# Performance work log

Measured on AMD Instinct MI355X. Metric: run time of the kernel, lower is better.

Reference implementation:

```python
import jax, jax.numpy as jnp
import numpy as np

LN_EPS = 1e-6          # flax nn.LayerNorm default
ATTN_EPS = 1e-9        # numerical_stabilizer default


def ln_points(x, scale, bias):
    """flax LayerNorm(reduction_axes=-2): stats over points axis, affine over feature axis."""
    mu = jnp.mean(x, axis=-2, keepdims=True)
    var = jnp.mean(jnp.square(x), axis=-2, keepdims=True) - jnp.square(mu)
    return (x - mu) * jax.lax.rsqrt(var + LN_EPS) * scale + bias


def self_attention_layer(x, wq_i, bq_i, wk_i, bk_i, wv_i, bv_i, wo_i, bo_i, ls_i, lb_i):
    # 1x1 convs == pointwise linears
    q = x @ wq_i + bq_i                                  # [B,N,C]
    k = x @ wk_i + bk_i
    v = x @ wv_i + bv_i
    attn = jnp.einsum('bmc,bnc->bmn', q, k)              # [B,M,N]
    attn = jax.nn.softmax(attn, axis=-1)
    # extra offset-attention renorm: divide by column sums (axis=1)
    attn = attn / (ATTN_EPS + jnp.sum(attn, axis=1, keepdims=True))
    # einsum '...MN,...NC->...NC' reduces M: scales v by column sums
    col = jnp.sum(attn, axis=1)                          # [B,N]
    out = col[..., None] * v                             # [B,N,C]
    out = out @ wo_i + bo_i
    out = jax.nn.relu(ln_points(out, ls_i, lb_i))
    return out + x


def setup_inputs() -> dict:
    key = jax.random.key(0)
    ks = jax.random.split(key, 16)
    B, N, IN, C, F, L = 2, 4096, 3, 256, 1024, 4
    s_in = 1.0 / np.sqrt(IN)
    s_c = 1.0 / np.sqrt(C)
    s_f = 1.0 / np.sqrt(L * C)
    return {
        'inputs': jax.random.normal(ks[0], (B, N, IN), jnp.float32),
        'w0': jax.random.normal(ks[1], (IN, C), jnp.float32) * s_in,
        'b0': jnp.zeros((C,), jnp.float32),
        'ln0_s': jnp.ones((C,), jnp.float32),
        'ln0_b': jnp.zeros((C,), jnp.float32),
        'w1': jax.random.normal(ks[2], (C, C), jnp.float32) * s_c,
        'b1': jnp.zeros((C,), jnp.float32),
        'ln1_s': jnp.ones((C,), jnp.float32),
        'ln1_b': jnp.zeros((C,), jnp.float32),
        'wq': jax.random.normal(ks[3], (L, C, C), jnp.float32) * s_c,
        'bq': jnp.zeros((L, C), jnp.float32),
        'wk': jax.random.normal(ks[4], (L, C, C), jnp.float32) * s_c,
        'bk': jnp.zeros((L, C), jnp.float32),
        'wv': jax.random.normal(ks[5], (L, C, C), jnp.float32) * s_c,
        'bv': jnp.zeros((L, C), jnp.float32),
        'wo': jax.random.normal(ks[6], (L, C, C), jnp.float32) * s_c,
        'bo': jnp.zeros((L, C), jnp.float32),
        'attn_ln_s': jnp.ones((L, C), jnp.float32),
        'attn_ln_b': jnp.zeros((L, C), jnp.float32),
        'wf': jax.random.normal(ks[7], (L * C, F), jnp.float32) * s_f,
        'bf': jnp.zeros((F,), jnp.float32),
    }


def reference(inputs, w0, b0, ln0_s, ln0_b, w1, b1, ln1_s, ln1_b,
              wq, bq, wk, bk, wv, bv, wo, bo, attn_ln_s, attn_ln_b, wf, bf):
    # pre-conv stack
    out = ln_points(inputs @ w0 + b0, ln0_s, ln0_b)
    out = ln_points(out @ w1 + b1, ln1_s, ln1_b)
    # attention stack (4 structurally identical layers, concatenated)
    attn_outs = []
    for i in range(wq.shape[0]):
        out = self_attention_layer(out, wq[i], bq[i], wk[i], bk[i],
                                   wv[i], bv[i], wo[i], bo[i],
                                   attn_ln_s[i], attn_ln_b[i])
        attn_outs.append(out)
    out = jnp.concatenate(attn_outs, axis=-1)            # [B,N,4C]
    out = out @ wf + bf                                  # [B,N,F]
    return out
```

## Files before the change

### kernel.cpp

```cpp
#include <hip/hip_runtime.h>

#define BB 2
#define NN 4096
#define CC 256
#define FF 1024
#define NLAYER 4
#define RR (BB*NN)
#define SPL 16
#define QKLD (3*CC)
#define NEG_BIG (-1e30f)
#define LOG2E 1.44269504f

typedef _Float16 h16;
typedef __attribute__((ext_vector_type(8))) _Float16 half8;
typedef __attribute__((ext_vector_type(4))) float f32x4;
typedef __attribute__((ext_vector_type(16))) float f32x16;

#define WAITVM4 asm volatile("s_waitcnt vmcnt(4)" ::: "memory")
#define WAITVM0 asm volatile("s_waitcnt vmcnt(0)" ::: "memory")

__device__ __forceinline__ void gload16(const h16* g, h16* l) {
    __builtin_amdgcn_global_load_lds((const __attribute__((address_space(1))) void*)g,
                                     (__attribute__((address_space(3))) void*)l, 16, 0, 0);
}

template<int ROWS>
__device__ __forceinline__ void stage_rows(const h16* __restrict__ src, int ld,
    int row0, int c0, h16* lds, int tid)
{
    int w = tid >> 6;
    #pragma unroll
    for (int t = 0; t < ROWS/32; ++t) {
        int slot = t*256 + tid;
        int row = slot >> 3;
        int pp  = slot & 7;
        int piece = pp ^ (row & 7);
        gload16(src + (size_t)(row0 + row)*ld + c0 + piece*8,
                lds + (t*256 + w*64)*8);
    }
}

__device__ __forceinline__ half8 frag_ld(const h16* lds, int row, int pl) {
    return *(const half8*)(lds + row*64 + ((pl ^ (row & 7))*8));
}

__global__ __launch_bounds__(256) void pct_wtrans(const float* __restrict__ W,
    h16* __restrict__ WT, int K, int N, int dstride, float scale)
{
    __shared__ h16 t[32][33];
    const float* Wl = W + (size_t)blockIdx.z*K*N;
    h16* WTl = WT + (size_t)blockIdx.z*dstride;
    int k0 = blockIdx.x*32, n0 = blockIdx.y*32;
    int tx = threadIdx.x & 31, ty = threadIdx.x >> 5;
    #pragma unroll
    for (int i = ty; i < 32; i += 8)
        t[i][tx] = (h16)(Wl[(size_t)(k0+i)*N + n0 + tx] * scale);
    __syncthreads();
    #pragma unroll
    for (int i = ty; i < 32; i += 8)
        WTl[(size_t)(n0+i)*K + k0 + tx] = t[tx][i];
}

__global__ __launch_bounds__(256) void pct_wtrans_qkv(const float* __restrict__ wq,
    const float* __restrict__ wk, const float* __restrict__ wv, h16* __restrict__ WT)
{
    __shared__ h16 t[32][33];
    int z = blockIdx.z;
    int which = z >> 2, layer = z & 3;
    const float* Wl = (which == 0 ? wq : which == 1 ? wk : wv) + (size_t)layer*CC*CC;
    h16* WTl = WT + (size_t)layer*QKLD*CC + (size_t)which*CC*CC;
    float scale = (which == 0) ? LOG2E : 1.0f;
    int k0 = blockIdx.x*32, n0 = blockIdx.y*32;
    int tx = threadIdx.x & 31, ty = threadIdx.x >> 5;
    #pragma unroll
    for (int i = ty; i < 32; i += 8)
        t[i][tx] = (h16)(Wl[(size_t)(k0+i)*CC + n0 + tx] * scale);
    __syncthreads();
    #pragma unroll
    for (int i = ty; i < 32; i += 8)
        WTl[(size_t)(n0+i)*CC + k0 + tx] = t[tx][i];
}

__global__ __launch_bounds__(256) void pct_bias3(const float* __restrict__ bq,
    const float* __restrict__ bk, const float* __restrict__ bv, float* __restrict__ o)
{
    int l = blockIdx.x, c = threadIdx.x;
    o[l*QKLD + c]        = bq[l*CC + c] * LOG2E;
    o[l*QKLD + CC + c]   = bk[l*CC + c];
    o[l*QKLD + 2*CC + c] = bv[l*CC + c];
}

__global__ __launch_bounds__(256) void pct_embed(const float* __restrict__ inp,
    const float* __restrict__ w0, const float* __restrict__ b0,
    h16* __restrict__ out, float* __restrict__ sums)
{
    int c = threadIdx.x;
    int r0 = blockIdx.x * 64;
    float wa = w0[c], wb = w0[CC+c], wcv = w0[2*CC+c], bb = b0[c];
    float s1 = 0.f, s2 = 0.f;
    #pragma unroll 4
    for (int i = 0; i < 64; ++i) {
        int r = r0 + i;
        float y = bb + inp[r*3+0]*wa + inp[r*3+1]*wb + inp[r*3+2]*wcv;
        h16 hy = (h16)y;
        out[(size_t)r*CC + c] = hy;
        float yf = (float)hy;
        s1 += yf; s2 += yf*yf;
    }
    int b = r0 >> 12;
    atomicAdd(&sums[((size_t)b*CC + c)*2 + 0], s1);
    atomicAdd(&sums[((size_t)b*CC + c)*2 + 1], s2);
}

__global__ __launch_bounds__(256) void pct_lnapply(const h16* __restrict__ x, int ldx,
    const float* __restrict__ sums, const float* __restrict__ scale, const float* __restrict__ bias,
    const h16* __restrict__ res, int ldr, h16* __restrict__ out, int ldo,
    int do_relu)
{
    int r = blockIdx.x*8 + (threadIdx.x >> 5);
    int cg = (threadIdx.x & 31) * 8;
    int b = r / NN;
    half8 xv = *(const half8*)(x + (size_t)r*ldx + cg);
    half8 rv;
    if (res) rv = *(const half8*)(res + (size_t)r*ldr + cg);
    half8 ov;
    #pragma unroll
    for (int j = 0; j < 8; ++j) {
        int c = cg + j;
        float s1 = sums[(b*CC + c)*2], s2 = sums[(b*CC + c)*2 + 1];
        float mu  = s1 * (1.f/NN);
        float var = s2 * (1.f/NN) - mu*mu;
        float rstd = rsqrtf(var + 1e-6f);
        float y = ((float)xv[j] - mu) * rstd * scale[c] + bias[c];
        if (do_relu) y = fmaxf(y, 0.f);
        if (res) y += (float)rv[j];
        ov[j] = (h16)y;
    }
    *(half8*)(out + (size_t)r*ldo + cg) = ov;
}

template<int BN, bool OUT_F32, bool CSTAT>
__global__ __launch_bounds__(256) void pct_gemm_f16(
    const h16* __restrict__ A, int lda,
    const h16* __restrict__ WT, const float* __restrict__ bias,
    void* __restrict__ outp, int ldo, int K, const float* __restrict__ rowS,
    float* __restrict__ csums)
{
    constexpr int BJ = BN/2;
    constexpr int NF = BJ/16;
    __shared__ __align__(16) h16 Asm[128*64];
    __shared__ __align__(16) h16 Bsm[BN*64];
    const int tid = threadIdx.x;
    const int lane = tid & 63, w = tid >> 6;
    const int ln = lane & 15, lq = lane >> 4;
    const int wr = w >> 1, wc = w & 1;
    const int m0 = blockIdx.x*128, n0 = blockIdx.y*BN;
    f32x4 acc[4][NF];
    #pragma unroll
    for (int i = 0; i < 4; ++i)
        #pragma unroll
        for (int j = 0; j < NF; ++j) acc[i][j] = (f32x4){0.f,0.f,0.f,0.f};
    for (int k0 = 0; k0 < K; k0 += 64) {
        stage_rows<128>(A, lda, m0, k0, Asm, tid);
        stage_rows<BN>(WT, K, n0, k0, Bsm, tid);
        __syncthreads();
        #pragma unroll
        for (int kk = 0; kk < 2; ++kk) {
            half8 af[4], bfr[NF];
            #pragma unroll
            for (int i = 0; i < 4; ++i) af[i] = frag_ld(Asm, wr*64 + i*16 + ln, kk*4 + lq);
            #pragma unroll
            for (int j = 0; j < NF; ++j) bfr[j] = frag_ld(Bsm, wc*BJ + j*16 + ln, kk*4 + lq);
            #pragma unroll
            for (int i = 0; i < 4; ++i)
                #pragma unroll
                for (int j = 0; j < NF; ++j)
                    acc[i][j] = __builtin_amdgcn_mfma_f32_16x16x32_f16(af[i], bfr[j], acc[i][j], 0, 0, 0);
        }
        __syncthreads();
    }
    float cs1[NF], cs2[NF];
    #pragma unroll
    for (int j = 0; j < NF; ++j) {
        int col = n0 + wc*BJ + j*16 + ln;
        float bv = bias[col];
        float s1 = 0.f, s2 = 0.f;
        #pragma unroll
        for (int i = 0; i < 4; ++i) {
            #pragma unroll
            for (int r = 0; r < 4; ++r) {
                int row = m0 + wr*64 + i*16 + lq*4 + r;
                float sc = 1.f;
                if (rowS) { float s = rowS[row]; sc = s / (1e-9f + s); }
                float v = acc[i][j][r] * sc + bv;
                if (OUT_F32) ((float*)outp)[(size_t)row*ldo + col] = v;
                else ((h16*)outp)[(size_t)row*ldo + col] = (h16)v;
                if (CSTAT) { s1 += v; s2 += v*v; }
            }
        }
        cs1[j] = s1; cs2[j] = s2;
    }
    if constexpr (CSTAT) {
        __shared__ float cred[2][2][BJ][2];
        #pragma unroll
        for (int j = 0; j < NF; ++j) {
            float s1 = cs1[j], s2 = cs2[j];
            s1 += __shfl_down(s1, 16); s1 += __shfl_down(s1, 32);
            s2 += __shfl_down(s2, 16); s2 += __shfl_down(s2, 32);
            if (lane < 16) {
                cred[wr][wc][j*16 + lane][0] = s1;
                cred[wr][wc][j*16 + lane][1] = s2;
            }
        }
        __syncthreads();
        if (tid < 2*BN) {
            int c = tid >> 1, st = tid & 1;
            int wcc = c >> 5, ci = c & 31;
            float v = cred[0][wcc][ci][st] + cred[1][wcc][ci][st];
            int b = m0 >> 12;
            atomicAdd(&csums[((size_t)b*CC + n0 + c)*2 + st], v);
        }
    }
}

__global__ __launch_bounds__(256) void attn_rowstats(const h16* __restrict__ QKV,
    float2* __restrict__ part)
{
    __shared__ __align__(16) h16 Ks[3*128*64];
    const int b = blockIdx.x, mt = blockIdx.y, sp = blockIdx.z;
    const int tid = threadIdx.x;
    const int lane = tid & 63, w = tid >> 6;
    const int ln2 = lane & 31, h = lane >> 5;
    const h16* qb = QKV + (size_t)b*NN*QKLD;
    const h16* kb = qb + CC;
    const int m0 = mt*128;
    const h16* qrow = qb + (size_t)(m0 + w*32 + ln2)*QKLD + h*8;
    half8 qreg[16];
    #pragma unroll
    for (int i = 0; i < 16; ++i) qreg[i] = *(const half8*)(qrow + i*16);

    const int nbeg = sp*(NN/SPL);
    constexpr int NT = (NN/SPL)/128;
    constexpr int NCH = NT*4;
    float rm = NEG_BIG, rs = 0.f;

    stage_rows<128>(kb, QKLD, nbeg, 0, Ks, tid);
    stage_rows<128>(kb, QKLD, nbeg, 64, Ks + 8192, tid);
    int id = 0;
    #pragma unroll
    for (int t = 0; t < NT; ++t) {
        f32x16 acc[4];
        #pragma unroll
        for (int j = 0; j < 4; ++j) acc[j] = (f32x16)(0.f);
        #pragma unroll
        for (int c = 0; c < 4; ++c, ++id) {
            if (id == NCH-1) { WAITVM0; } else { WAITVM4; }
            __builtin_amdgcn_s_barrier();
            if (id + 2 < NCH)
                stage_rows<128>(kb, QKLD, nbeg + ((id+2) >> 2)*128, ((id+2) & 3)*64,
                                Ks + ((id+2) % 3)*8192, tid);
            const h16* buf = Ks + (id % 3)*8192;
            __builtin_amdgcn_s_setprio(1);
            #pragma unroll
            for (int kk = 0; kk < 4; ++kk) {
                half8 bq = qreg[c*4 + kk];
                #pragma unroll
                for (int j = 0; j < 4; ++j) {
                    half8 af = frag_ld(buf, j*32 + ln2, kk*2 + h);
                    acc[j] = __builtin_amdgcn_mfma_f32_32x32x16_f16(af, bq, acc[j], 0, 0, 0);
                }
            }
            __builtin_amdgcn_s_setprio(0);
        }
        float tm = NEG_BIG;
        #pragma unroll
        for (int j = 0; j < 4; ++j)
            #pragma unroll
            for (int g = 0; g < 16; g += 2)
                tm = fmaxf(tm, fmaxf(acc[j][g], acc[j][g+1]));
        if (tm > rm) { rs *= exp2f(rm - tm); rm = tm; }
        float s = 0.f;
        #pragma unroll
        for (int j = 0; j < 4; ++j)
            #pragma unroll
            for (int g = 0; g < 16; ++g)
                s += exp2f(acc[j][g] - rm);
        rs += s;
    }
    float mo = __shfl_xor(rm, 32, 64);
    float so = __shfl_xor(rs, 32, 64);
    float mn = fmaxf(rm, mo);
    float sm = rs*exp2f(rm - mn) + so*exp2f(mo - mn);
    if (lane < 32) {
        int m = m0 + w*32 + ln2;
        part[((size_t)b*NN + m)*SPL + sp] = make_float2(mn, sm);
    }
}

__global__ __launch_bounds__(256) void attn_colsums(const h16* __restrict__ QKV,
    const float2* __restrict__ part, float* __restrict__ S)
{
    __shared__ __align__(16) h16 Qs[3*128*64];
    __shared__ float2 rst_s[256];
    const int b = blockIdx.x, nt = blockIdx.y, sp = blockIdx.z;
    const int tid = threadIdx.x;
    const int lane = tid & 63, w = tid >> 6;
    const int ln2 = lane & 31, h = lane >> 5;
    const h16* qb = QKV + (size_t)b*NN*QKLD;
    const h16* kb = qb + CC;
    const int n0 = nt*128;
    const int mbeg = sp*(NN/SPL);

    {
        const float2* pp = part + ((size_t)b*NN + mbeg + tid)*SPL;
        float m = NEG_BIG;
        #pragma unroll
        for (int s = 0; s < SPL; ++s) m = fmaxf(m, pp[s].x);
        float sum = 0.f;
        #pragma unroll
        for (int s = 0; s < SPL; ++s) sum += pp[s].y * exp2f(pp[s].x - m);
        rst_s[tid] = make_float2(m, 1.0f / sum);
    }
    __syncthreads();

    const h16* krow = kb + (size_t)(n0 + w*32 + ln2)*QKLD + h*8;
    half8 kreg[16];
    #pragma unroll
    for (int i = 0; i < 16; ++i) kreg[i] = *(const half8*)(krow + i*16);

    constexpr int NT = (NN/SPL)/128;
    constexpr int NCH = NT*4;
    float cs = 0.f;

    stage_rows<128>(qb, QKLD, mbeg, 0, Qs, tid);
    stage_rows<128>(qb, QKLD, mbeg, 64, Qs + 8192, tid);
    int id = 0;
    #pragma unroll
    for (int t = 0; t < NT; ++t) {
        f32x16 acc[4];
        #pragma unroll
        for (int j = 0; j < 4; ++j) acc[j] = (f32x16)(0.f);
        #pragma unroll
        for (int c = 0; c < 4; ++c, ++id) {
            if (id == NCH-1) { WAITVM0; } else { WAITVM4; }
            __builtin_amdgcn_s_barrier();
            if (id + 2 < NCH)
                stage_rows<128>(qb, QKLD, mbeg + ((id+2) >> 2)*128, ((id+2) & 3)*64,
                                Qs + ((id+2) % 3)*8192, tid);
            const h16* buf = Qs + (id % 3)*8192;
            __builtin_amdgcn_s_setprio(1);
            #pragma unroll
            for (int kk = 0; kk < 4; ++kk) {
                half8 bk = kreg[c*4 + kk];
                #pragma unroll
                for (int j = 0; j < 4; ++j) {
                    half8 af = frag_ld(buf, j*32 + ln2, kk*2 + h);
                    acc[j] = __builtin_amdgcn_mfma_f32_32x32x16_f16(af, bk, acc[j], 0, 0, 0);
                }
            }
            __builtin_amdgcn_s_setprio(0);
        }
        int mt0 = t*128;
        #pragma unroll
        for (int j = 0; j < 4; ++j) {
            #pragma unroll
            for (int g = 0; g < 16; ++g) {
                int mloc = mt0 + j*32 + (g & 3) + 8*(g >> 2) + 4*h;
                float2 st = rst_s[mloc];
                cs += exp2f(acc[j][g] - st.x) * st.y;
            }
        }
    }
    cs += __shfl_xor(cs, 32, 64);
    if (lane < 32) {
        int n = n0 + w*32 + ln2;
        atomicAdd(&S[(size_t)b*NN + n], cs);
    }
}

extern "C" void kernel_launch(void* const* d_in, const int* in_sizes, int n_in,
                              void* d_out, int out_size, void* d_ws, size_t ws_size,
                              hipStream_t stream)
{
    const float* inp  = (const float*)d_in[0];
    const float* w0   = (const float*)d_in[1];
    const float* b0   = (const float*)d_in[2];
    const float* ln0s = (const float*)d_in[3];
    const float* ln0b = (const float*)d_in[4];
    const float* w1   = (const float*)d_in[5];
    const float* b1   = (const float*)d_in[6];
    const float* ln1s = (const float*)d_in[7];
    const float* ln1b = (const float*)d_in[8];
    const float* wq   = (const float*)d_in[9];
    const float* bq   = (const float*)d_in[10];
    const float* wk   = (const float*)d_in[11];
    const float* bk   = (const float*)d_in[12];
    const float* wv   = (const float*)d_in[13];
    const float* bv   = (const float*)d_in[14];
    const float* wo   = (const float*)d_in[15];
    const float* bo   = (const float*)d_in[16];
    const float* alns = (const float*)d_in[17];
    const float* alnb = (const float*)d_in[18];
    const float* wf   = (const float*)d_in[19];
    const float* bfb  = (const float*)d_in[20];
    float* out = (float*)d_out;

    char* p = (char*)d_ws;
    auto alloc = [&](size_t bytes) { char* r = p; p += (bytes + 255) & ~255ULL; return r; };
    h16* t0    = (h16*)alloc((size_t)RR*CC*2);
    h16* t1    = (h16*)alloc((size_t)RR*CC*2);
    h16* t2    = (h16*)alloc((size_t)RR*CC*2);
    h16* x1    = (h16*)alloc((size_t)RR*CC*2);
    h16* qkv   = (h16*)alloc((size_t)RR*QKLD*2);
    h16* oh    = (h16*)alloc((size_t)RR*CC*2);
    h16* xcat  = (h16*)alloc((size_t)RR*FF*2);
    h16* w1T   = (h16*)alloc((size_t)CC*CC*2);
    h16* wqkvT = (h16*)alloc((size_t)NLAYER*QKLD*CC*2);
    h16* woT   = (h16*)alloc((size_t)NLAYER*CC*CC*2);
    h16* wfT   = (h16*)alloc((size_t)FF*FF*2);
    float* bqkv  = (float*)alloc((size_t)NLAYER*QKLD*4);
    float2* part  = (float2*)alloc((size_t)RR*SPL*8);
    float* Ssum  = (float*)alloc((size_t)NLAYER*RR*4);
    float* lns   = (float*)alloc((size_t)6*BB*CC*2*4);

    dim3 blk(256);

    hipMemsetAsync(Ssum, 0, (size_t)((char*)(lns + 6*BB*CC*2) - (char*)Ssum), stream);

    pct_wtrans<<<dim3(CC/32, CC/32, 1), blk, 0, stream>>>(w1, w1T, CC, CC, CC*CC, 1.f);
    pct_wtrans_qkv<<<dim3(CC/32, CC/32, 3*NLAYER), blk, 0, stream>>>(wq, wk, wv, wqkvT);
    pct_wtrans<<<dim3(CC/32, CC/32, NLAYER), blk, 0, stream>>>(wo, woT, CC, CC, CC*CC, 1.f);
    pct_wtrans<<<dim3(FF/32, FF/32, 1), blk, 0, stream>>>(wf, wfT, FF, FF, FF*FF, 1.f);
    pct_bias3<<<NLAYER, blk, 0, stream>>>(bq, bk, bv, bqkv);

    pct_embed<<<RR/64, blk, 0, stream>>>(inp, w0, b0, t0, lns + 0*BB*CC*2);
    pct_lnapply<<<RR/8, blk, 0, stream>>>(t0, CC, lns + 0*BB*CC*2, ln0s, ln0b, nullptr, 0, t1, CC, 0);
    pct_gemm_f16<64,false,true><<<dim3(RR/128, CC/64), blk, 0, stream>>>(
        t1, CC, w1T, b1, t2, CC, CC, nullptr, lns + 1*BB*CC*2);
    pct_lnapply<<<RR/8, blk, 0, stream>>>(t2, CC, lns + 1*BB*CC*2, ln1s, ln1b, nullptr, 0, x1, CC, 0);

    const h16* xin = x1; int ldx = CC;
    for (int i = 0; i < NLAYER; ++i) {
        pct_gemm_f16<64,false,false><<<dim3(RR/128, QKLD/64), blk, 0, stream>>>(
            xin, ldx, wqkvT + (size_t)i*QKLD*CC, bqkv + i*QKLD, qkv, QKLD, CC, nullptr, nullptr);

        attn_rowstats<<<dim3(BB, NN/128, SPL), blk, 0, stream>>>(qkv, part);
        attn_colsums<<<dim3(BB, NN/128, SPL), blk, 0, stream>>>(qkv, part, Ssum + (size_t)i*RR);

        pct_gemm_f16<64,false,true><<<dim3(RR/128, CC/64), blk, 0, stream>>>(
            qkv + 2*CC, QKLD, woT + (size_t)i*CC*CC, bo + i*CC, oh, CC, CC,
            Ssum + (size_t)i*RR, lns + (2+i)*BB*CC*2);

        pct_lnapply<<<RR/8, blk, 0, stream>>>(oh, CC, lns + (2+i)*BB*CC*2, alns + i*CC, alnb + i*CC,
                                              xin, ldx, xcat + i*CC, FF, 1);
        xin = xcat + i*CC; ldx = FF;
    }

    pct_gemm_f16<128,true,false><<<dim3(RR/128, FF/128), blk, 0, stream>>>(
        xcat, FF, wfT, bfb, out, FF, FF, nullptr, nullptr);
}
```

Before: 498.6 us.

## Store fp16 attention scores in rowstats and reuse them for column sums

The row-statistics kernel now writes every QK^T logit tile to a global fp16 scores buffer. A new column-sum kernel reads that buffer back instead of recomputing the second QK^T matmul with staged Q tiles. It applies the row max and inverse sum, reduces each column with wave shuffles and LDS, and adds the result atomically. This trades the recomputed matmul for a large extra write and read of scores per layer, plus many shuffles, and lowers logit precision to fp16 before the exponential. The wait counts in rowstats are adjusted to account for the new stores.

New measurement: 549.2 us. +10.2%, slower.

```diff
diff --git a/kernel.cpp b/kernel.cpp
--- a/kernel.cpp
+++ b/kernel.cpp
@@ -12,12 +12,12 @@
 #define LOG2E 1.44269504f
 
 typedef _Float16 h16;
+typedef __attribute__((ext_vector_type(4))) _Float16 half4;
 typedef __attribute__((ext_vector_type(8))) _Float16 half8;
 typedef __attribute__((ext_vector_type(4))) float f32x4;
 typedef __attribute__((ext_vector_type(16))) float f32x16;
 
-#define WAITVM4 asm volatile("s_waitcnt vmcnt(4)" ::: "memory")
-#define WAITVM0 asm volatile("s_waitcnt vmcnt(0)" ::: "memory")
+#define WAITVM(n) asm volatile("s_waitcnt vmcnt(" #n ")" ::: "memory")
 
 __device__ __forceinline__ void gload16(const h16* g, h16* l) {
     __builtin_amdgcn_global_load_lds((const __attribute__((address_space(1))) void*)g,
@@ -224,7 +224,7 @@
 }
 
 __global__ __launch_bounds__(256) void attn_rowstats(const h16* __restrict__ QKV,
-    float2* __restrict__ part)
+    float2* __restrict__ part, h16* __restrict__ scores)
 {
     __shared__ __align__(16) h16 Ks[3*128*64];
     const int b = blockIdx.x, mt = blockIdx.y, sp = blockIdx.z;
@@ -254,7 +254,9 @@
         for (int j = 0; j < 4; ++j) acc[j] = (f32x16)(0.f);
         #pragma unroll
         for (int c = 0; c < 4; ++c, ++id) {
-            if (id == NCH-1) { WAITVM0; } else { WAITVM4; }
+            if (id == NCH-1)      { WAITVM(0); }
+            else if (t > 0 && c < 2) { WAITVM(20); }
+            else                  { WAITVM(4); }
             __builtin_amdgcn_s_barrier();
             if (id + 2 < NCH)
                 stage_rows<128>(kb, QKLD, nbeg + ((id+2) >> 2)*128, ((id+2) & 3)*64,
@@ -272,6 +274,18 @@
             }
             __builtin_amdgcn_s_setprio(0);
         }
+        {
+            size_t tb = (((((size_t)b*32 + mt)*16 + sp)*4 + w)*2 + t)*4096;
+            #pragma unroll
+            for (int j = 0; j < 4; ++j) {
+                #pragma unroll
+                for (int q = 0; q < 4; ++q) {
+                    half4 pk = { (h16)acc[j][4*q+0], (h16)acc[j][4*q+1],
+                                 (h16)acc[j][4*q+2], (h16)acc[j][4*q+3] };
+                    *(half4*)(scores + tb + (size_t)(j*4+q)*256 + lane*4) = pk;
+                }
+            }
+        }
         float tm = NEG_BIG;
         #pragma unroll
         for (int j = 0; j < 4; ++j)
@@ -297,22 +311,18 @@
     }
 }
 
-__global__ __launch_bounds__(256) void attn_colsums(const h16* __restrict__ QKV,
+__global__ __launch_bounds__(256) void attn_colsum2(const h16* __restrict__ scores,
     const float2* __restrict__ part, float* __restrict__ S)
 {
-    __shared__ __align__(16) h16 Qs[3*128*64];
-    __shared__ float2 rst_s[256];
-    const int b = blockIdx.x, nt = blockIdx.y, sp = blockIdx.z;
+    __shared__ float2 rst_s[128];
+    __shared__ float colred[4][256];
+    const int b = blockIdx.x, mt = blockIdx.y, sp = blockIdx.z;
     const int tid = threadIdx.x;
     const int lane = tid & 63, w = tid >> 6;
     const int ln2 = lane & 31, h = lane >> 5;
-    const h16* qb = QKV + (size_t)b*NN*QKLD;
-    const h16* kb = qb + CC;
-    const int n0 = nt*128;
-    const int mbeg = sp*(NN/SPL);
-
-    {
-        const float2* pp = part + ((size_t)b*NN + mbeg + tid)*SPL;
+
+    if (tid < 128) {
+        const float2* pp = part + ((size_t)b*NN + mt*128 + tid)*SPL;
         float m = NEG_BIG;
         #pragma unroll
         for (int s = 0; s < SPL; ++s) m = fmaxf(m, pp[s].x);
@@ -322,60 +332,46 @@
         rst_s[tid] = make_float2(m, 1.0f / sum);
     }
     __syncthreads();
-
-    const h16* krow = kb + (size_t)(n0 + w*32 + ln2)*QKLD + h*8;
-    half8 kreg[16];
-    #pragma unroll
-    for (int i = 0; i < 16; ++i) kreg[i] = *(const half8*)(krow + i*16);
-
-    constexpr int NT = (NN/SPL)/128;
-    constexpr int NCH = NT*4;
-    float cs = 0.f;
-
-    stage_rows<128>(qb, QKLD, mbeg, 0, Qs, tid);
-    stage_rows<128>(qb, QKLD, mbeg, 64, Qs + 8192, tid);
-    int id = 0;
-    #pragma unroll
-    for (int t = 0; t < NT; ++t) {
-        f32x16 acc[4];
-        #pragma unroll
-        for (int j = 0; j < 4; ++j) acc[j] = (f32x16)(0.f);
-        #pragma unroll
-        for (int c = 0; c < 4; ++c, ++id) {
-            if (id == NCH-1) { WAITVM0; } else { WAITVM4; }
-            __builtin_amdgcn_s_barrier();
-            if (id + 2 < NCH)
-                stage_rows<128>(qb, QKLD, mbeg + ((id+2) >> 2)*128, ((id+2) & 3)*64,
-                                Qs + ((id+2) % 3)*8192, tid);
-            const h16* buf = Qs + (id % 3)*8192;
-            __builtin_amdgcn_s_setprio(1);
-            #pragma unroll
-            for (int kk = 0; kk < 4; ++kk) {
-                half8 bk = kreg[c*4 + kk];
+    float2 st = rst_s[w*32 + ln2];
+    const float mx = st.x, ri = st.y;
+
+    half4 vv[2][16];
+    #pragma unroll
+    for (int t = 0; t < 2; ++t) {
+        size_t tb = (((((size_t)b*32 + mt)*16 + sp)*4 + w)*2 + t)*4096;
+        #pragma unroll
+        for (int s = 0; s < 16; ++s)
+            vv[t][s] = *(const half4*)(scores + tb + (size_t)s*256 + lane*4);
+    }
+    #pragma unroll
+    for (int t = 0; t < 2; ++t) {
+        #pragma unroll
+        for (int j = 0; j < 4; ++j) {
+            #pragma unroll
+            for (int q = 0; q < 4; ++q) {
+                half4 v = vv[t][j*4+q];
+                float s0 = exp2f((float)v[0] - mx) * ri;
+                float s1 = exp2f((float)v[1] - mx) * ri;
+                float s2 = exp2f((float)v[2] - mx) * ri;
+                float s3 = exp2f((float)v[3] - mx) * ri;
                 #pragma unroll
-                for (int j = 0; j < 4; ++j) {
-                    half8 af = frag_ld(buf, j*32 + ln2, kk*2 + h);
-                    acc[j] = __builtin_amdgcn_mfma_f32_32x32x16_f16(af, bk, acc[j], 0, 0, 0);
+                for (int d = 1; d < 32; d <<= 1) {
+                    s0 += __shfl_xor(s0, d, 64);
+                    s1 += __shfl_xor(s1, d, 64);
+                    s2 += __shfl_xor(s2, d, 64);
+                    s3 += __shfl_xor(s3, d, 64);
+                }
+                if (ln2 == 0) {
+                    int nb = t*128 + j*32 + q*8 + 4*h;
+                    colred[w][nb+0] = s0; colred[w][nb+1] = s1;
+                    colred[w][nb+2] = s2; colred[w][nb+3] = s3;
                 }
             }
-            __builtin_amdgcn_s_setprio(0);
-        }
-        int mt0 = t*128;
-        #pragma unroll
-        for (int j = 0; j < 4; ++j) {
-            #pragma unroll
-            for (int g = 0; g < 16; ++g) {
-                int mloc = mt0 + j*32 + (g & 3) + 8*(g >> 2) + 4*h;
-                float2 st = rst_s[mloc];
-                cs += exp2f(acc[j][g] - st.x) * st.y;
-            }
-        }
-    }
-    cs += __shfl_xor(cs, 32, 64);
-    if (lane < 32) {
-        int n = n0 + w*32 + ln2;
-        atomicAdd(&S[(size_t)b*NN + n], cs);
-    }
+        }
+    }
+    __syncthreads();
+    atomicAdd(&S[(size_t)b*NN + sp*256 + tid],
+              colred[0][tid] + colred[1][tid] + colred[2][tid] + colred[3][tid]);
 }
 
 extern "C" void kernel_launch(void* const* d_in, const int* in_sizes, int n_in,
@@ -422,6 +418,7 @@
     float2* part  = (float2*)alloc((size_t)RR*SPL*8);
     float* Ssum  = (float*)alloc((size_t)NLAYER*RR*4);
     float* lns   = (float*)alloc((size_t)6*BB*CC*2*4);
+    h16* scoreb = (h16*)alloc((size_t)RR*NN*2);
 
     dim3 blk(256);
 
@@ -444,8 +441,8 @@
         pct_gemm_f16<64,false,false><<<dim3(RR/128, QKLD/64), blk, 0, stream>>>(
             xin, ldx, wqkvT + (size_t)i*QKLD*CC, bqkv + i*QKLD, qkv, QKLD, CC, nullptr, nullptr);
 
-        attn_rowstats<<<dim3(BB, NN/128, SPL), blk, 0, stream>>>(qkv, part);
-        attn_colsums<<<dim3(BB, NN/128, SPL), blk, 0, stream>>>(qkv, part, Ssum + (size_t)i*RR);
+        attn_rowstats<<<dim3(BB, NN/128, SPL), blk, 0, stream>>>(qkv, part, scoreb);
+        attn_colsum2<<<dim3(BB, NN/128, SPL), blk, 0, stream>>>(scoreb, part, Ssum + (size_t)i*RR);
 
         pct_gemm_f16<64,false,true><<<dim3(RR/128, CC/64), blk, 0, stream>>>(
             qkv + 2*CC, QKLD, woT + (size_t)i*CC*CC, bo + i*CC, oh, CC, CC,
```
